# Optimization experiments

Hardware: AMD Instinct MI355X
Metric: run time of the kernel (lower is better)

The kernel has to match this reference:

```python
import jax, jax.numpy as jnp
import numpy as np

B, L, P = 2, 1024, 1024
HID = 2048
NH, NKV, D = 32, 8, 64
T = P + L
N_REPEAT = NH // NKV
SCALE = D ** -0.5
NEG_INF = -1e9


def _rotate_half(x):
    x1, x2 = jnp.split(x, 2, axis=-1)
    return jnp.concatenate([-x2, x1], axis=-1)


def _apply_rope(q, k, cos, sin):
    # cos/sin: [L, D] -> broadcast to [1, 1, L, D]
    cos = cos[None, None, :, :]
    sin = sin[None, None, :, :]
    q = q * cos + _rotate_half(q) * sin
    k = k * cos + _rotate_half(k) * sin
    return q, k


def setup_inputs() -> dict:
    key = jax.random.key(0)
    ks = jax.random.split(key, 10)
    s = 0.02
    x = jax.random.normal(ks[0], (B, L, HID), jnp.float32)
    Wq = jax.random.normal(ks[1], (HID, NH * D), jnp.float32) * s
    bq = jnp.zeros((NH * D,), jnp.float32)
    Wk = jax.random.normal(ks[2], (HID, NKV * D), jnp.float32) * s
    bk = jnp.zeros((NKV * D,), jnp.float32)
    Wv = jax.random.normal(ks[3], (HID, NKV * D), jnp.float32) * s
    bv = jnp.zeros((NKV * D,), jnp.float32)
    Wo = jax.random.normal(ks[4], (NH * D, HID), jnp.float32) * s
    past_k = jax.random.normal(ks[5], (B, NKV, P, D), jnp.float32)
    past_v = jax.random.normal(ks[6], (B, NKV, P, D), jnp.float32)
    # RoPE tables for the L new positions (offsets P..P+L-1)
    pos = jnp.arange(P, P + L, dtype=jnp.float32)
    inv_freq = 1.0 / (10000.0 ** (jnp.arange(0, D, 2, dtype=jnp.float32) / D))
    freqs = pos[:, None] * inv_freq[None, :]            # [L, D/2]
    emb = jnp.concatenate([freqs, freqs], axis=-1)       # [L, D]
    cos = jnp.cos(emb)
    sin = jnp.sin(emb)
    # causal additive mask over total kv length T (past always visible)
    i = jnp.arange(L)[:, None]
    j = jnp.arange(T)[None, :]
    m = jnp.where(j <= i + P, 0.0, NEG_INF).astype(jnp.float32)  # [L, T]
    attention_mask = jnp.broadcast_to(m[None, None], (B, 1, L, T))
    return {
        "x": x, "attention_mask": attention_mask, "cos": cos, "sin": sin,
        "past_k": past_k, "past_v": past_v,
        "Wq": Wq, "bq": bq, "Wk": Wk, "bk": bk, "Wv": Wv, "bv": bv, "Wo": Wo,
    }


def reference(x, attention_mask, cos, sin, past_k, past_v, Wq, bq, Wk, bk, Wv, bv, Wo):
    # QKV projections
    q = (x @ Wq + bq).reshape(B, L, NH, D).transpose(0, 2, 1, 3)    # [B,NH,L,D]
    k = (x @ Wk + bk).reshape(B, L, NKV, D).transpose(0, 2, 1, 3)   # [B,NKV,L,D]
    v = (x @ Wv + bv).reshape(B, L, NKV, D).transpose(0, 2, 1, 3)
    q, k = _apply_rope(q, k, cos, sin)
    # KV-cache append
    k = jnp.concatenate([past_k, k], axis=2)  # [B,NKV,T,D]
    v = jnp.concatenate([past_v, v], axis=2)
    # repeat_kv for GQA
    if N_REPEAT > 1:
        k = jnp.repeat(k, N_REPEAT, axis=1)   # [B,NH,T,D]
        v = jnp.repeat(v, N_REPEAT, axis=1)
    w = jnp.einsum("bhld,bhtd->bhlt", q, k) * SCALE
    w = w + attention_mask
    w = jax.nn.softmax(w, axis=-1)
    out = jnp.einsum("bhlt,bhtd->bhld", w, v)
    out = out.transpose(0, 2, 1, 3).reshape(B, L, NH * D)
    return out @ Wo
```

## Files before the change

kernel.cpp:

```cpp
#include <hip/hip_runtime.h>
#include <stdint.h>

#define Bc   2
#define Lc   1024
#define Pc   1024
#define Tc   2048
#define HIDc 2048
#define NHc  32
#define NKVc 8
#define Dc   64

typedef __bf16 bf16x8 __attribute__((ext_vector_type(8)));
typedef float f32x4 __attribute__((ext_vector_type(4)));
typedef float f32x16 __attribute__((ext_vector_type(16)));

__device__ inline unsigned short f2bf(float f) {
  union { float f; uint32_t u; } v; v.f = f;
  uint32_t u = v.u;
  uint32_t r = (u + 0x7fffu + ((u >> 16) & 1u)) >> 16;
  return (unsigned short)r;
}
__device__ inline float bf2f(unsigned short h) {
  union { uint32_t u; float f; } v; v.u = ((uint32_t)h) << 16;
  return v.f;
}
__device__ inline float exp2_fast(float x) {
#if defined(__has_builtin)
#if __has_builtin(__builtin_amdgcn_exp2f)
  return __builtin_amdgcn_exp2f(x);
#else
  return exp2f(x);
#endif
#else
  return exp2f(x);
#endif
}
__device__ inline unsigned int cvtpk_bf16(float a, float b) {
  unsigned int r;
  asm("v_cvt_pk_bf16_f32 %0, %1, %2" : "=v"(r) : "v"(a), "v"(b));
  return r;
}
__device__ inline void plane32_swap(unsigned int& a, unsigned int& b) {
  asm("v_permlane32_swap_b32 %0, %1" : "+v"(a), "+v"(b));
}

typedef const __attribute__((address_space(1))) unsigned int* gas1_t;
typedef __attribute__((address_space(3))) unsigned int* las3_t;
__device__ inline void gload_lds16(const void* g, void* l) {
  __builtin_amdgcn_global_load_lds((gas1_t)g, (las3_t)l, 16, 0, 0);
}

__global__ void prep_kernel(const float* __restrict__ x, unsigned short* __restrict__ xb,
                            const float* __restrict__ Wq, const float* __restrict__ Wk,
                            const float* __restrict__ Wv, const float* __restrict__ Wo,
                            unsigned short* __restrict__ WqkvT,
                            unsigned short* __restrict__ WoT) {
  __shared__ float s[32][33];
  const int tid = threadIdx.x;
  if (blockIdx.x < 4096) {
    int i = (blockIdx.x * 256 + tid) * 4;
    float4 v = *(const float4*)(x + i);
    ushort4 o;
    o.x = f2bf(v.x); o.y = f2bf(v.y); o.z = f2bf(v.z); o.w = f2bf(v.w);
    *(ushort4*)(xb + i) = o;
    return;
  }
  int bx2 = blockIdx.x - 4096;
  int bx = bx2 % 160;
  int k0 = (bx2 / 160) * 32;
  const float* W;
  unsigned short* dst;
  int N, n0, drow;
  if (bx < 64)       { W = Wq; dst = WqkvT; N = 2048; n0 = bx * 32;        drow = n0; }
  else if (bx < 80)  { W = Wk; dst = WqkvT; N = 512;  n0 = (bx - 64) * 32; drow = 2048 + n0; }
  else if (bx < 96)  { W = Wv; dst = WqkvT; N = 512;  n0 = (bx - 80) * 32; drow = 2560 + n0; }
  else               { W = Wo; dst = WoT;   N = 2048; n0 = (bx - 96) * 32; drow = n0; }
  int tx = tid & 31, ty = tid >> 5;
#pragma unroll
  for (int j = 0; j < 4; ++j)
    s[ty + j * 8][tx] = W[(size_t)(k0 + ty + j * 8) * N + n0 + tx];
  __syncthreads();
#pragma unroll
  for (int j = 0; j < 4; ++j)
    dst[(size_t)(drow + ty + j * 8) * 2048 + k0 + tx] = f2bf(s[tx][ty + j * 8]);
}

template <int TM, bool OUT_F32>
__global__ __launch_bounds__(256, 2) void gemm_kernel(
    const unsigned short* __restrict__ A, const unsigned short* __restrict__ BT,
    const float* __restrict__ bq, const float* __restrict__ bk, const float* __restrict__ bv,
    void* __restrict__ Cout, int N) {
  const int K = 2048;
  const int MI = TM / 32;
  __shared__ unsigned short sA[2][TM * 32];
  __shared__ unsigned short sB[2][128 * 32];
  const int m0 = blockIdx.y * TM, n0 = blockIdx.x * 128;
  const int tid = threadIdx.x;
  const int lane = tid & 63, w = tid >> 6;
  const int l15 = lane & 15, quad = lane >> 4;
  const int wm = (w & 1) * (TM / 2), wn = (w >> 1) * 64;

  f32x4 acc[MI][4];
#pragma unroll
  for (int i = 0; i < MI; ++i)
#pragma unroll
    for (int j = 0; j < 4; ++j) {
      f32x4 z = {0.f, 0.f, 0.f, 0.f};
      acc[i][j] = z;
    }

  const unsigned short* ga = A + (size_t)(m0 + (tid >> 2)) * K + (tid & 3) * 8;
  const unsigned short* gb = BT + (size_t)(n0 + (tid >> 2)) * K + (tid & 3) * 8;

  auto issue = [&](int tile, int buf) {
    int kb = tile * 32;
#pragma unroll
    for (int i = 0; i < TM / 64; ++i)
      gload_lds16(ga + (size_t)(i * 64) * K + kb, &sA[buf][i * 64 * 32 + tid * 8]);
    gload_lds16(gb + kb, &sB[buf][tid * 8]);
    gload_lds16(gb + (size_t)64 * K + kb, &sB[buf][64 * 32 + tid * 8]);
  };

  issue(0, 0);
  for (int t = 0; t < 64; ++t) {
    int tn = (t + 1 < 64) ? t + 1 : 63;
    issue(tn, (t + 1) & 1);
    if (TM == 128)
      asm volatile("s_waitcnt vmcnt(4)" ::: "memory");
    else
      asm volatile("s_waitcnt vmcnt(3)" ::: "memory");
    __builtin_amdgcn_s_barrier();
    const unsigned short* bA = sA[t & 1];
    const unsigned short* bB = sB[t & 1];
    bf16x8 af[MI], bfr[4];
#pragma unroll
    for (int i = 0; i < MI; ++i)
      af[i] = *(const bf16x8*)(bA + (wm + i * 16 + l15) * 32 + quad * 8);
#pragma unroll
    for (int i = 0; i < 4; ++i)
      bfr[i] = *(const bf16x8*)(bB + (wn + i * 16 + l15) * 32 + quad * 8);
#pragma unroll
    for (int mi = 0; mi < MI; ++mi)
#pragma unroll
      for (int ni = 0; ni < 4; ++ni)
        acc[mi][ni] = __builtin_amdgcn_mfma_f32_16x16x32_bf16(af[mi], bfr[ni], acc[mi][ni], 0, 0, 0);
    asm volatile("s_waitcnt lgkmcnt(0)" ::: "memory");
    __builtin_amdgcn_s_barrier();
  }

#pragma unroll
  for (int mi = 0; mi < MI; ++mi)
#pragma unroll
    for (int ni = 0; ni < 4; ++ni) {
      int col = n0 + wn + ni * 16 + l15;
      float bvv = 0.f;
      if (bq) bvv = (col < 2048) ? bq[col] : (col < 2560 ? bk[col - 2048] : bv[col - 2560]);
#pragma unroll
      for (int r = 0; r < 4; ++r) {
        int row = m0 + wm + mi * 16 + quad * 4 + r;
        float v = acc[mi][ni][r] + bvv;
        if (OUT_F32)
          ((float*)Cout)[(size_t)row * N + col] = v;
        else
          ((unsigned short*)Cout)[(size_t)row * N + col] = f2bf(v);
      }
    }
}

__global__ void build_kv_kernel(const unsigned short* __restrict__ qkv,
                                const float* __restrict__ past_k,
                                const float* __restrict__ past_v,
                                const float* __restrict__ cosb, const float* __restrict__ sinb,
                                unsigned short* __restrict__ Kc,
                                unsigned short* __restrict__ Vc) {
  __shared__ __align__(16) unsigned short sK[64 * 72];
  __shared__ __align__(16) unsigned short sVT[64 * 72];
  union U8 { bf16x8 v; unsigned short u[8]; };

  const int bid = blockIdx.x;
  const int bh = bid >> 5, tt = bid & 31;
  const int b = bh >> 3, hk = bh & 7;
  const int tid = threadIdx.x;
  const int tl = tid >> 2;
  const int c16 = (tid & 3) * 16;

  const int t = tt * 64 + tl;

  U8 ko0, ko1;
  if (tt < 16) {
    const float* src = past_k + (((size_t)bh * 1024 + t) * 64 + c16);
#pragma unroll
    for (int i = 0; i < 8; ++i) ko0.u[i] = f2bf(src[i]);
#pragma unroll
    for (int i = 0; i < 8; ++i) ko1.u[i] = f2bf(src[8 + i]);
  } else {
    const int l = t - 1024;
    const unsigned short* krow = qkv + ((size_t)(b * 1024 + l)) * 3072 + 2048 + hk * 64;
    const int po = (c16 < 32) ? 32 : -32;
    const float sgn = (c16 < 32) ? -1.f : 1.f;
    U8 own0, own1, par0, par1;
    own0.v = *(const bf16x8*)(krow + c16);
    own1.v = *(const bf16x8*)(krow + c16 + 8);
    par0.v = *(const bf16x8*)(krow + c16 + po);
    par1.v = *(const bf16x8*)(krow + c16 + po + 8);
    const float* cb = cosb + l * 64 + c16;
    const float* sb = sinb + l * 64 + c16;
#pragma unroll
    for (int i = 0; i < 8; ++i)
      ko0.u[i] = f2bf(bf2f(own0.u[i]) * cb[i] + sgn * bf2f(par0.u[i]) * sb[i]);
#pragma unroll
    for (int i = 0; i < 8; ++i)
      ko1.u[i] = f2bf(bf2f(own1.u[i]) * cb[8 + i] + sgn * bf2f(par1.u[i]) * sb[8 + i]);
  }
  *(bf16x8*)&sK[tl * 72 + c16] = ko0.v;
  *(bf16x8*)&sK[tl * 72 + c16 + 8] = ko1.v;

  if (tt < 16) {
    const float* src = past_v + (((size_t)bh * 1024 + t) * 64 + c16);
#pragma unroll
    for (int i = 0; i < 16; ++i) sVT[(c16 + i) * 72 + tl] = f2bf(src[i]);
  } else {
    const unsigned short* vrow = qkv + ((size_t)(b * 1024 + (t - 1024))) * 3072 + 2560 + hk * 64 + c16;
    U8 v0, v1;
    v0.v = *(const bf16x8*)(vrow);
    v1.v = *(const bf16x8*)(vrow + 8);
#pragma unroll
    for (int i = 0; i < 8; ++i) sVT[(c16 + i) * 72 + tl] = v0.u[i];
#pragma unroll
    for (int i = 0; i < 8; ++i) sVT[(c16 + 8 + i) * 72 + tl] = v1.u[i];
  }

  __syncthreads();

  unsigned short* KD = Kc + (size_t)bh * 131072 + (size_t)tt * 4096;
  unsigned short* VD = Vc + (size_t)bh * 131072 + (size_t)tt * 4096;
#pragma unroll
  for (int half = 0; half < 2; ++half) {
    int c = tid + half * 256;
    int f = c >> 6, l = c & 63;
    int col = (f & 3) * 16 + (l >> 5) * 8;
    int row = (f >> 2) * 32 + (l & 31);
    *(bf16x8*)(KD + f * 512 + l * 8) = *(const bf16x8*)&sK[row * 72 + col];
    *(bf16x8*)(VD + f * 512 + l * 8) = *(const bf16x8*)&sVT[row * 72 + col];
  }
}

__global__ __launch_bounds__(256, 4) void attn_kernel(
    const unsigned short* __restrict__ qkv,
    const unsigned short* __restrict__ Kc,
    const unsigned short* __restrict__ Vc,
    const float* __restrict__ cosb, const float* __restrict__ sinb,
    unsigned short* __restrict__ O) {
  __shared__ __align__(16) char smraw[35328];
  unsigned short* vst = (unsigned short*)smraw;
  float (*comb)[32][68] = (float (*)[32][68])smraw;
  float* lsmem = (float*)(smraw + 34816);

  const int flat = blockIdx.x;
  const int hk = flat & 7;
  const int b = (flat >> 3) & 1;
  const int h2 = (flat >> 4) & 3;
  const int qt = 31 - (flat >> 6);
  const int h = hk * 4 + h2;
  const int q0 = qt * 32;
  const int bh = b * 8 + hk;

  const int tid = threadIdx.x;
  const int lane = tid & 63, w = tid >> 6;
  const int l31 = lane & 31, hh = lane >> 5;

  union U8 { bf16x8 v; unsigned short u[8]; };
  union PB { unsigned int w4[4]; bf16x8 v; };

  const unsigned short* KT = Kc + (size_t)bh * 131072;
  const unsigned short* VT = Vc + (size_t)bh * 131072;
  unsigned short* vwave = vst + w * 4096;

  const float SC = 0.125f * 1.44269504f;
  bf16x8 qB[4];
  {
    int row = q0 + l31;
    const unsigned short* qrow = qkv + (size_t)(b * 1024 + row) * 3072 + h * 64;
    U8 raw[4];
#pragma unroll
    for (int ks = 0; ks < 4; ++ks)
      raw[ks].v = *(const bf16x8*)(qrow + ks * 16 + hh * 8);
#pragma unroll
    for (int ks = 0; ks < 2; ++ks) {
      int dbase = ks * 16 + hh * 8;
      float4 ca = *(const float4*)(cosb + row * 64 + dbase);
      float4 cb = *(const float4*)(cosb + row * 64 + dbase + 4);
      float4 sa = *(const float4*)(sinb + row * 64 + dbase);
      float4 sb = *(const float4*)(sinb + row * 64 + dbase + 4);
      float c[8] = {ca.x, ca.y, ca.z, ca.w, cb.x, cb.y, cb.z, cb.w};
      float sn[8] = {sa.x, sa.y, sa.z, sa.w, sb.x, sb.y, sb.z, sb.w};
      U8 flo, fhi;
#pragma unroll
      for (int j = 0; j < 8; ++j) {
        float ql = bf2f(raw[ks].u[j]), qh = bf2f(raw[ks + 2].u[j]);
        float cc = c[j] * SC, ss = sn[j] * SC;
        flo.u[j] = f2bf(ql * cc - qh * ss);
        fhi.u[j] = f2bf(qh * cc + ql * ss);
      }
      qB[ks] = flo.v;
      qB[ks + 2] = fhi.v;
    }
  }

  f32x16 oaccT[2];
  {
    f32x16 z;
#pragma unroll
    for (int i = 0; i < 16; ++i) z[i] = 0.f;
    oaccT[0] = z; oaccT[1] = z;
  }
  float lsum = 0.f;

  const int ntile = (q0 + 1119) >> 6;

  for (int kt = w; kt < ntile; kt += 4) {
    asm volatile("" ::: "memory");
    const unsigned short* vb = VT + (size_t)kt * 4096 + lane * 8;
#pragma unroll
    for (int f = 0; f < 8; ++f)
      gload_lds16(vb + f * 512, vwave + f * 512);

    const unsigned short* kb = KT + (size_t)kt * 4096 + lane * 8;
    bf16x8 kf[8];
#pragma unroll
    for (int f = 0; f < 8; ++f) kf[f] = *(const bf16x8*)(kb + f * 512);

    f32x16 sacc[2];
    {
      f32x16 z;
#pragma unroll
      for (int i = 0; i < 16; ++i) z[i] = 0.f;
      sacc[0] = z; sacc[1] = z;
    }
#pragma unroll
    for (int ks = 0; ks < 4; ++ks)
      sacc[0] = __builtin_amdgcn_mfma_f32_32x32x16_bf16(kf[ks], qB[ks], sacc[0], 0, 0, 0);
#pragma unroll
    for (int ks = 0; ks < 4; ++ks)
      sacc[1] = __builtin_amdgcn_mfma_f32_32x32x16_bf16(kf[4 + ks], qB[ks], sacc[1], 0, 0, 0);

    const int t0 = kt * 64;
    unsigned int pk[2][8];
    const bool diag = (t0 + 63 > q0 + Pc);
    if (!diag) {
#pragma unroll
      for (int mf = 0; mf < 2; ++mf)
#pragma unroll
        for (int p = 0; p < 8; ++p) {
          float e0 = exp2_fast(sacc[mf][2 * p]);
          float e1 = exp2_fast(sacc[mf][2 * p + 1]);
          lsum += e0 + e1;
          pk[mf][p] = cvtpk_bf16(e0, e1);
        }
    } else {
      int rg = q0 + l31 + Pc;
#pragma unroll
      for (int mf = 0; mf < 2; ++mf)
#pragma unroll
        for (int p = 0; p < 8; ++p) {
          int r0 = 2 * p;
          int tg = t0 + mf * 32 + (r0 & 3) + 8 * (r0 >> 2) + 4 * hh;
          float e0 = (tg <= rg) ? exp2_fast(sacc[mf][r0]) : 0.f;
          float e1 = (tg + 1 <= rg) ? exp2_fast(sacc[mf][r0 + 1]) : 0.f;
          lsum += e0 + e1;
          pk[mf][p] = cvtpk_bf16(e0, e1);
        }
    }

    PB pb[4];
#pragma unroll
    for (int ks = 0; ks < 4; ++ks) {
      int mf = ks >> 1, o = (ks & 1) * 4;
      unsigned int a0 = pk[mf][o + 0], b0 = pk[mf][o + 2];
      unsigned int a1 = pk[mf][o + 1], b1 = pk[mf][o + 3];
      plane32_swap(a0, b0);
      plane32_swap(a1, b1);
      pb[ks].w4[0] = a0; pb[ks].w4[1] = a1; pb[ks].w4[2] = b0; pb[ks].w4[3] = b1;
    }

    asm volatile("s_waitcnt vmcnt(0)" ::: "memory");
    bf16x8 vf[8];
#pragma unroll
    for (int f = 0; f < 8; ++f)
      vf[f] = *(const bf16x8*)(vwave + f * 512 + lane * 8);

#pragma unroll
    for (int md = 0; md < 2; ++md)
#pragma unroll
      for (int ks = 0; ks < 4; ++ks)
        oaccT[md] = __builtin_amdgcn_mfma_f32_32x32x16_bf16(vf[md * 4 + ks], pb[ks].v, oaccT[md], 0, 0, 0);
  }

  __syncthreads();
  lsum += __shfl_xor(lsum, 32);
  if (hh == 0) lsmem[w * 32 + l31] = lsum;
#pragma unroll
  for (int md = 0; md < 2; ++md)
#pragma unroll
    for (int g = 0; g < 4; ++g) {
      float4 fv = {oaccT[md][4 * g + 0], oaccT[md][4 * g + 1],
                   oaccT[md][4 * g + 2], oaccT[md][4 * g + 3]};
      *(float4*)&comb[w][l31][md * 32 + 8 * g + 4 * hh] = fv;
    }
  __syncthreads();

  const int q = tid >> 3, c8 = (tid & 7) * 8;
  float a8[8];
#pragma unroll
  for (int i = 0; i < 8; ++i) a8[i] = 0.f;
#pragma unroll
  for (int wv = 0; wv < 4; ++wv) {
    float4 p0 = *(const float4*)&comb[wv][q][c8];
    float4 p1 = *(const float4*)&comb[wv][q][c8 + 4];
    a8[0] += p0.x; a8[1] += p0.y; a8[2] += p0.z; a8[3] += p0.w;
    a8[4] += p1.x; a8[5] += p1.y; a8[6] += p1.z; a8[7] += p1.w;
  }
  float linv = 1.f / (lsmem[0 * 32 + q] + lsmem[1 * 32 + q] + lsmem[2 * 32 + q] + lsmem[3 * 32 + q]);
  uint4 ov;
  ov.x = cvtpk_bf16(a8[0] * linv, a8[1] * linv);
  ov.y = cvtpk_bf16(a8[2] * linv, a8[3] * linv);
  ov.z = cvtpk_bf16(a8[4] * linv, a8[5] * linv);
  ov.w = cvtpk_bf16(a8[6] * linv, a8[7] * linv);
  int row = b * 1024 + q0 + q;
  *(uint4*)(O + (size_t)row * 2048 + h * 64 + c8) = ov;
}

extern "C" void kernel_launch(void* const* d_in, const int* in_sizes, int n_in,
                              void* d_out, int out_size, void* d_ws, size_t ws_size,
                              hipStream_t stream) {
  const float* x      = (const float*)d_in[0];
  const float* cosb   = (const float*)d_in[2];
  const float* sinb   = (const float*)d_in[3];
  const float* past_k = (const float*)d_in[4];
  const float* past_v = (const float*)d_in[5];
  const float* Wq     = (const float*)d_in[6];
  const float* bq     = (const float*)d_in[7];
  const float* Wk     = (const float*)d_in[8];
  const float* bk     = (const float*)d_in[9];
  const float* Wv     = (const float*)d_in[10];
  const float* bv     = (const float*)d_in[11];
  const float* Wo     = (const float*)d_in[12];
  float* out = (float*)d_out;

  char* ws = (char*)d_ws;
  unsigned short* xb    = (unsigned short*)(ws + ((size_t)0 << 20));
  unsigned short* WqkvT = (unsigned short*)(ws + ((size_t)8 << 20));
  unsigned short* WoT   = (unsigned short*)(ws + ((size_t)20 << 20));
  unsigned short* qkvb  = (unsigned short*)(ws + ((size_t)28 << 20));
  unsigned short* Kc    = (unsigned short*)(ws + ((size_t)40 << 20));
  unsigned short* Vc    = (unsigned short*)(ws + ((size_t)44 << 20));
  unsigned short* attno = (unsigned short*)(ws + ((size_t)48 << 20));

  prep_kernel<<<14336, 256, 0, stream>>>(x, xb, Wq, Wk, Wv, Wo, WqkvT, WoT);

  gemm_kernel<64, false><<<dim3(24, 32), 256, 0, stream>>>(xb, WqkvT, bq, bk, bv, qkvb, 3072);

  build_kv_kernel<<<512, 256, 0, stream>>>(qkvb, past_k, past_v, cosb, sinb, Kc, Vc);

  attn_kernel<<<2048, 256, 0, stream>>>(qkvb, Kc, Vc, cosb, sinb, attno);

  gemm_kernel<64, true><<<dim3(16, 32), 256, 0, stream>>>(attno, WoT, nullptr, nullptr, nullptr, out, 2048);
}
```

Measured before the change: 259.7 us.

## Load V directly to registers and shrink LDS to raise attention occupancy

Removes the per-wave LDS staging of V tiles (global-to-LDS async loads plus vmcnt wait) and instead loads V fragments straight into registers after the softmax. The cross-wave output combine is split into two 32-column halves, so the shared buffer shrinks from about 35 KB to about 20 KB. Launch bounds are raised to 8 blocks per SM so more waves can hide latency. The cost is more register pressure under a tighter register cap, and V loads no longer overlap the QK MFMA and exp work.

```diff
diff --git a/kernel.cpp b/kernel.cpp
--- a/kernel.cpp
+++ b/kernel.cpp
@@ -245,16 +245,14 @@
   }
 }
 
-__global__ __launch_bounds__(256, 4) void attn_kernel(
+__global__ __launch_bounds__(256, 8) void attn_kernel(
     const unsigned short* __restrict__ qkv,
     const unsigned short* __restrict__ Kc,
     const unsigned short* __restrict__ Vc,
     const float* __restrict__ cosb, const float* __restrict__ sinb,
     unsigned short* __restrict__ O) {
-  __shared__ __align__(16) char smraw[35328];
-  unsigned short* vst = (unsigned short*)smraw;
-  float (*comb)[32][68] = (float (*)[32][68])smraw;
-  float* lsmem = (float*)(smraw + 34816);
+  __shared__ float comb[4][32][36];
+  __shared__ float lsmem[4][32];
 
   const int flat = blockIdx.x;
   const int hk = flat & 7;
@@ -274,7 +272,6 @@
 
   const unsigned short* KT = Kc + (size_t)bh * 131072;
   const unsigned short* VT = Vc + (size_t)bh * 131072;
-  unsigned short* vwave = vst + w * 4096;
 
   const float SC = 0.125f * 1.44269504f;
   bf16x8 qB[4];
@@ -319,12 +316,6 @@
   const int ntile = (q0 + 1119) >> 6;
 
   for (int kt = w; kt < ntile; kt += 4) {
-    asm volatile("" ::: "memory");
-    const unsigned short* vb = VT + (size_t)kt * 4096 + lane * 8;
-#pragma unroll
-    for (int f = 0; f < 8; ++f)
-      gload_lds16(vb + f * 512, vwave + f * 512);
-
     const unsigned short* kb = KT + (size_t)kt * 4096 + lane * 8;
     bf16x8 kf[8];
 #pragma unroll
@@ -372,6 +363,11 @@
         }
     }
 
+    const unsigned short* vb = VT + (size_t)kt * 4096 + lane * 8;
+    bf16x8 vf[8];
+#pragma unroll
+    for (int f = 0; f < 8; ++f) vf[f] = *(const bf16x8*)(vb + f * 512);
+
     PB pb[4];
 #pragma unroll
     for (int ks = 0; ks < 4; ++ks) {
@@ -383,12 +379,6 @@
       pb[ks].w4[0] = a0; pb[ks].w4[1] = a1; pb[ks].w4[2] = b0; pb[ks].w4[3] = b1;
     }
 
-    asm volatile("s_waitcnt vmcnt(0)" ::: "memory");
-    bf16x8 vf[8];
-#pragma unroll
-    for (int f = 0; f < 8; ++f)
-      vf[f] = *(const bf16x8*)(vwave + f * 512 + lane * 8);
-
 #pragma unroll
     for (int md = 0; md < 2; ++md)
 #pragma unroll
@@ -396,38 +386,32 @@
         oaccT[md] = __builtin_amdgcn_mfma_f32_32x32x16_bf16(vf[md * 4 + ks], pb[ks].v, oaccT[md], 0, 0, 0);
   }
 
-  __syncthreads();
   lsum += __shfl_xor(lsum, 32);
-  if (hh == 0) lsmem[w * 32 + l31] = lsum;
-#pragma unroll
-  for (int md = 0; md < 2; ++md)
+  if (hh == 0) lsmem[w][l31] = lsum;
+  const int q = tid >> 3, c4 = (tid & 7) * 4;
+  const int row = b * 1024 + q0 + q;
+#pragma unroll
+  for (int md = 0; md < 2; ++md) {
+    __syncthreads();
 #pragma unroll
     for (int g = 0; g < 4; ++g) {
       float4 fv = {oaccT[md][4 * g + 0], oaccT[md][4 * g + 1],
                    oaccT[md][4 * g + 2], oaccT[md][4 * g + 3]};
-      *(float4*)&comb[w][l31][md * 32 + 8 * g + 4 * hh] = fv;
-    }
-  __syncthreads();
-
-  const int q = tid >> 3, c8 = (tid & 7) * 8;
-  float a8[8];
-#pragma unroll
-  for (int i = 0; i < 8; ++i) a8[i] = 0.f;
-#pragma unroll
-  for (int wv = 0; wv < 4; ++wv) {
-    float4 p0 = *(const float4*)&comb[wv][q][c8];
-    float4 p1 = *(const float4*)&comb[wv][q][c8 + 4];
-    a8[0] += p0.x; a8[1] += p0.y; a8[2] += p0.z; a8[3] += p0.w;
-    a8[4] += p1.x; a8[5] += p1.y; a8[6] += p1.z; a8[7] += p1.w;
-  }
-  float linv = 1.f / (lsmem[0 * 32 + q] + lsmem[1 * 32 + q] + lsmem[2 * 32 + q] + lsmem[3 * 32 + q]);
-  uint4 ov;
-  ov.x = cvtpk_bf16(a8[0] * linv, a8[1] * linv);
-  ov.y = cvtpk_bf16(a8[2] * linv, a8[3] * linv);
-  ov.z = cvtpk_bf16(a8[4] * linv, a8[5] * linv);
-  ov.w = cvtpk_bf16(a8[6] * linv, a8[7] * linv);
-  int row = b * 1024 + q0 + q;
-  *(uint4*)(O + (size_t)row * 2048 + h * 64 + c8) = ov;
+      *(float4*)&comb[w][l31][8 * g + 4 * hh] = fv;
+    }
+    __syncthreads();
+    float4 a4 = {0.f, 0.f, 0.f, 0.f};
+#pragma unroll
+    for (int wv = 0; wv < 4; ++wv) {
+      float4 p = *(const float4*)&comb[wv][q][c4];
+      a4.x += p.x; a4.y += p.y; a4.z += p.z; a4.w += p.w;
+    }
+    float linv = 1.f / (lsmem[0][q] + lsmem[1][q] + lsmem[2][q] + lsmem[3][q]);
+    uint2 ov;
+    ov.x = cvtpk_bf16(a4.x * linv, a4.y * linv);
+    ov.y = cvtpk_bf16(a4.z * linv, a4.w * linv);
+    *(uint2*)(O + (size_t)row * 2048 + h * 64 + md * 32 + c4) = ov;
+  }
 }
 
 extern "C" void kernel_launch(void* const* d_in, const int* in_sizes, int n_in,
```

Result: slower. 464.2 us (+78.7%).
